# Performance work log

Hardware: AMD Instinct MI355X
Metric: run time of the kernel (lower is better)

## Reference

```python
import jax, jax.numpy as jnp
import numpy as np

N_HEAD = 16
HEAD_DIM = 32          # n_embed // n_head // 2
LAMBDA_INIT = 0.2      # 0.8 - 0.6*exp(-0.3*(layer-1)) with layer=1
ROPE_BASE = 10000.0
EPS = 1e-5


def _rope(x):
    # torchtune RotaryPositionalEmbeddings: interleaved adjacent pairs
    B, T, H, D = x.shape
    half = D // 2
    theta = ROPE_BASE ** (-(jnp.arange(half, dtype=jnp.float32) * 2.0 / D))  # [half]
    ang = jnp.arange(T, dtype=jnp.float32)[:, None] * theta[None, :]         # [T, half]
    cos = jnp.cos(ang)[None, :, None, :]
    sin = jnp.sin(ang)[None, :, None, :]
    xr = x.reshape(B, T, H, half, 2)
    x1, x2 = xr[..., 0], xr[..., 1]
    out = jnp.stack([x1 * cos - x2 * sin, x1 * sin + x2 * cos], axis=-1)
    return out.reshape(B, T, H, D).astype(x.dtype)


def reference(x, W_attn, W_proj, lambda_q1, lambda_k1, lambda_q2, lambda_k2):
    B, T, C = x.shape
    H, D = N_HEAD, HEAD_DIM
    qkv = x @ W_attn                              # [B,T,3C]
    q, k, v = jnp.split(qkv, 3, axis=-1)
    q = _rope(q.reshape(B, T, 2 * H, D)).transpose(0, 2, 1, 3)   # [B,2H,T,D]
    k = _rope(k.reshape(B, T, 2 * H, D)).transpose(0, 2, 1, 3)   # [B,2H,T,D]
    v = v.reshape(B, T, H, 2 * D).transpose(0, 2, 1, 3)          # [B,H,T,2D]

    lam = (jnp.exp(jnp.dot(lambda_q1, lambda_k1))
           - jnp.exp(jnp.dot(lambda_q2, lambda_k2)) + LAMBDA_INIT)

    # causal SDPA over both score paths (2H heads) in one pass, shared V
    scale = 1.0 / jnp.sqrt(jnp.asarray(D, x.dtype))
    scores = jnp.einsum('bhqd,bhkd->bhqk', q, k) * scale         # [B,2H,T,T]
    causal = jnp.tril(jnp.ones((T, T), dtype=bool))
    scores = jnp.where(causal, scores, jnp.finfo(scores.dtype).min)
    probs = jax.nn.softmax(scores, axis=-1)
    vv = jnp.concatenate([v, v], axis=1)                         # [B,2H,T,2D]
    A = jnp.einsum('bhqk,bhkd->bhqd', probs, vv)                 # [B,2H,T,2D]
    A1, A2 = A[:, :H], A[:, H:]

    diff = A1 - lam * A2                                         # [B,H,T,2D]
    # RMSNorm over last dim (2*head_dim), no affine, eps=1e-5
    diff = diff * jax.lax.rsqrt(jnp.mean(diff * diff, axis=-1, keepdims=True) + EPS)
    diff = (1.0 - LAMBDA_INIT) * diff
    out = diff.transpose(0, 2, 1, 3).reshape(B, T, C)
    return out @ W_proj


def setup_inputs() -> dict:
    key = jax.random.key(0)
    ks = jax.random.split(key, 7)
    B, T, C, D = 2, 2048, 1024, HEAD_DIM
    return {
        'x': jax.random.normal(ks[0], (B, T, C), jnp.float32),
        'W_attn': jax.random.normal(ks[1], (C, 3 * C), jnp.float32) * 0.02,
        'W_proj': jax.random.normal(ks[2], (C, C), jnp.float32) * 0.02,
        'lambda_q1': jax.random.normal(ks[3], (D,), jnp.float32) * 0.1,
        'lambda_k1': jax.random.normal(ks[4], (D,), jnp.float32) * 0.1,
        'lambda_q2': jax.random.normal(ks[5], (D,), jnp.float32) * 0.1,
        'lambda_k2': jax.random.normal(ks[6], (D,), jnp.float32) * 0.1,
    }
```

## Files before the change

### kernel.cpp

```cpp
#include <hip/hip_runtime.h>


typedef unsigned short u16;
typedef __bf16 bf16x8 __attribute__((ext_vector_type(8)));
typedef float f32x4 __attribute__((ext_vector_type(4)));
typedef float f32x16 __attribute__((ext_vector_type(16)));
typedef unsigned u32x2 __attribute__((ext_vector_type(2)));

__device__ __forceinline__ u16 f2bf(float f) {
  return __builtin_bit_cast(u16, (__bf16)f);
}
__device__ __forceinline__ float bf2f(u16 u) {
  return (float)__builtin_bit_cast(__bf16, u);
}
__device__ __forceinline__ unsigned pk2(float a, float b) {
  return (unsigned)f2bf(a) | ((unsigned)f2bf(b) << 16);
}

__device__ __forceinline__ void gload16(const u16* g, u16* l) {
  __builtin_amdgcn_global_load_lds(
      (const __attribute__((address_space(1))) unsigned int*)g,
      (__attribute__((address_space(3))) unsigned int*)l, 16, 0, 0);
}

__device__ __forceinline__ void trans_body(const float* __restrict__ in,
                                           u16* __restrict__ out, int R, int Cn,
                                           int bx, int by, float (*tile)[33],
                                           int tx, int ty) {
  const int c0 = bx * 32, r0 = by * 32;
#pragma unroll
  for (int rr = 0; rr < 4; ++rr)
    tile[ty + rr * 8][tx] = in[(size_t)(r0 + ty + rr * 8) * Cn + c0 + tx];
  __syncthreads();
#pragma unroll
  for (int rr = 0; rr < 4; ++rr)
    out[(size_t)(c0 + ty + rr * 8) * R + r0 + tx] = f2bf(tile[tx][ty + rr * 8]);
}

__global__ __launch_bounds__(256) void prep_kernel(
    const float* __restrict__ x, const float* __restrict__ Wa,
    const float* __restrict__ Wp, const float* __restrict__ lq1,
    const float* __restrict__ lk1, const float* __restrict__ lq2,
    const float* __restrict__ lk2, u16* __restrict__ xb, u16* __restrict__ WaT,
    u16* __restrict__ WpT, float2* __restrict__ Tab, float* __restrict__ lamp) {
  __shared__ float tile[32][33];
  const int id = blockIdx.x;
  const int tx = threadIdx.x & 31, ty = threadIdx.x >> 5;
  if (id < 4096) {
    const int i = id * 256 + threadIdx.x;
    float4 v = ((const float4*)x)[i];
    ushort4 o;
    o.x = f2bf(v.x); o.y = f2bf(v.y); o.z = f2bf(v.z); o.w = f2bf(v.w);
    ((ushort4*)xb)[i] = o;
  } else if (id < 7168) {
    const int t = id - 4096;
    trans_body(Wa, WaT, 1024, 3072, t % 96, t / 96, tile, tx, ty);
  } else if (id < 8192) {
    const int t = id - 7168;
    trans_body(Wp, WpT, 1024, 1024, t & 31, t >> 5, tile, tx, ty);
  } else if (id < 8320) {
    const int idx = (id - 8192) * 256 + threadIdx.x;
    const int t = idx >> 4, i = idx & 15;
    const float theta = exp2f(-0.83048202372184059f * (float)i);
    float sn, cs;
    sincosf((float)t * theta, &sn, &cs);
    Tab[idx] = make_float2(cs, sn);
  } else if (threadIdx.x == 0) {
    float d1 = 0.f, d2 = 0.f;
#pragma unroll
    for (int i = 0; i < 32; ++i) {
      d1 += lq1[i] * lk1[i];
      d2 += lq2[i] * lk2[i];
    }
    *lamp = expf(d1) - expf(d2) + 0.2f;
  }
}

__global__ __launch_bounds__(256, 6) void gemm_qkv_kernel(
    const u16* __restrict__ A, const u16* __restrict__ BT,
    u16* __restrict__ Q, u16* __restrict__ K, u16* __restrict__ VT,
    const float2* __restrict__ Tab) {
  const int Kdim = 1024;
  __shared__ u16 SH[12288];
  const int tid = threadIdx.x;
  const int l = tid & 63;
  const int w = tid >> 6;
  const int nwgx = gridDim.x;
  const int lin = blockIdx.x + nwgx * blockIdx.y;
  const int cpx = (nwgx * gridDim.y) >> 3;
  const int swz = (lin & 7) * cpx + (lin >> 3);
  const int bm = swz / nwgx, bn = swz % nwgx;
  const int wm = w >> 1, wn = w & 1;
  const int rowA0 = bm * 64, rowB0 = bn * 128;
  const int r_ = tid >> 2;
  const int s_ = (tid & 3) * 8;
  const u16* Ag = &A[(size_t)(rowA0 + r_) * Kdim + s_];
  const u16* Bg = &BT[(size_t)(rowB0 + r_) * Kdim + s_];
  const size_t rstride = (size_t)64 * Kdim;
  f32x4 acc[2][4] = {};
  gload16(Ag, &SH[tid * 8]);
  gload16(Bg, &SH[2048 + tid * 8]);
  gload16(Bg + rstride, &SH[4096 + tid * 8]);
  __syncthreads();
  int cur = 0;
  for (int t = 0; t < 32; ++t) {
    const u16* Asc = SH + cur * 6144;
    const u16* Bsc = Asc + 2048;
    if (t + 1 < 32) {
      u16* Asn = SH + (cur ^ 1) * 6144;
      const int k1 = (t + 1) * 32;
      gload16(Ag + k1, &Asn[tid * 8]);
      gload16(Bg + k1, &Asn[2048 + tid * 8]);
      gload16(Bg + rstride + k1, &Asn[4096 + tid * 8]);
    }
    bf16x8 a[2], b[4];
#pragma unroll
    for (int i = 0; i < 2; ++i)
      a[i] = *(const bf16x8*)&Asc[(wm * 32 + i * 16 + (l & 15)) * 32 + (l >> 4) * 8];
#pragma unroll
    for (int j = 0; j < 4; ++j)
      b[j] = *(const bf16x8*)&Bsc[(wn * 64 + j * 16 + (l & 15)) * 32 + (l >> 4) * 8];
    __builtin_amdgcn_s_setprio(1);
#pragma unroll
    for (int i = 0; i < 2; ++i)
#pragma unroll
      for (int j = 0; j < 4; ++j)
        acc[i][j] = __builtin_amdgcn_mfma_f32_16x16x32_bf16(a[i], b[j], acc[i][j], 0, 0, 0);
    __builtin_amdgcn_s_setprio(0);
    __syncthreads();
    cur ^= 1;
  }
  const int cr = (l >> 4) * 4;
  const int cc = l & 15;
  const int region = bn >> 3;
  const int b_ = rowA0 >> 11, tb = rowA0 & 2047;
  if (region < 2) {
    const float qsc_ = (region == 0) ? 0.25503486f : 1.0f;
    u16* dst = (region == 0) ? Q : K;
#pragma unroll
    for (int i = 0; i < 2; ++i) {
      const int trow0 = wm * 32 + i * 16 + cr;
#pragma unroll
      for (int j = 0; j < 4; ++j) {
        const int c = (bn & 7) * 128 + wn * 64 + j * 16 + cc;
        const int hh = c >> 5, d = c & 31;
        const int ii = d >> 1;
        const float sgn = (d & 1) ? 1.0f : -1.0f;
        const size_t base = (size_t)(b_ * 32 + hh) * 2048;
#pragma unroll
        for (int r = 0; r < 4; ++r) {
          const int t = tb + trow0 + r;
          const float2 cs = Tab[t * 16 + ii];
          const float xv = acc[i][j][r];
          const float px = __shfl_xor(xv, 1, 64);
          dst[(base + t) * 32 + d] = f2bf((xv * cs.x + sgn * px * cs.y) * qsc_);
        }
      }
    }
  } else {
#pragma unroll
    for (int i = 0; i < 2; ++i) {
      const int t0 = tb + wm * 32 + i * 16 + cr;
#pragma unroll
      for (int j = 0; j < 4; ++j) {
        const int c3 = (bn & 7) * 128 + wn * 64 + j * 16 + cc;
        const int hv = c3 >> 6, dv = c3 & 63;
        ushort4 ov;
        ov.x = f2bf(acc[i][j][0]);
        ov.y = f2bf(acc[i][j][1]);
        ov.z = f2bf(acc[i][j][2]);
        ov.w = f2bf(acc[i][j][3]);
        *(ushort4*)&VT[((size_t)(b_ * 16 + hv) * 64 + dv) * 2048 + t0] = ov;
      }
    }
  }
}

__global__ __launch_bounds__(256) void gemm_out_kernel(
    const u16* __restrict__ A, const u16* __restrict__ BT, float* __restrict__ Cout,
    int Mdim, int Ndim, int Kdim) {
  __shared__ u16 SH[12288];
  const int tid = threadIdx.x;
  const int l = tid & 63;
  const int w = tid >> 6;
  const int nwgx = gridDim.x;
  const int lin = blockIdx.x + nwgx * blockIdx.y;
  const int cpx = (nwgx * gridDim.y) >> 3;
  const int swz = (lin & 7) * cpx + (lin >> 3);
  const int bm = swz / nwgx, bn = swz % nwgx;
  const int wm = w >> 1, wn = w & 1;
  const int rowA0 = bm * 64, rowB0 = bn * 128;
  const int r_ = tid >> 2;
  const int s_ = (tid & 3) * 8;
  const u16* Ag = &A[(size_t)(rowA0 + r_) * Kdim + s_];
  const u16* Bg = &BT[(size_t)(rowB0 + r_) * Kdim + s_];
  const size_t rstride = (size_t)64 * Kdim;
  f32x4 acc[2][4] = {};
  gload16(Ag, &SH[tid * 8]);
  gload16(Bg, &SH[2048 + tid * 8]);
  gload16(Bg + rstride, &SH[4096 + tid * 8]);
  __syncthreads();
  int cur = 0;
  const int nt = Kdim >> 5;
  for (int t = 0; t < nt; ++t) {
    const u16* Asc = SH + cur * 6144;
    const u16* Bsc = Asc + 2048;
    if (t + 1 < nt) {
      u16* Asn = SH + (cur ^ 1) * 6144;
      const int k1 = (t + 1) * 32;
      gload16(Ag + k1, &Asn[tid * 8]);
      gload16(Bg + k1, &Asn[2048 + tid * 8]);
      gload16(Bg + rstride + k1, &Asn[4096 + tid * 8]);
    }
    bf16x8 a[2], b[4];
#pragma unroll
    for (int i = 0; i < 2; ++i)
      a[i] = *(const bf16x8*)&Asc[(wm * 32 + i * 16 + (l & 15)) * 32 + (l >> 4) * 8];
#pragma unroll
    for (int j = 0; j < 4; ++j)
      b[j] = *(const bf16x8*)&Bsc[(wn * 64 + j * 16 + (l & 15)) * 32 + (l >> 4) * 8];
    __builtin_amdgcn_s_setprio(1);
#pragma unroll
    for (int i = 0; i < 2; ++i)
#pragma unroll
      for (int j = 0; j < 4; ++j)
        acc[i][j] = __builtin_amdgcn_mfma_f32_16x16x32_bf16(a[i], b[j], acc[i][j], 0, 0, 0);
    __builtin_amdgcn_s_setprio(0);
    __syncthreads();
    cur ^= 1;
  }
  const int cr = (l >> 4) * 4;
  const int cc = l & 15;
#pragma unroll
  for (int i = 0; i < 2; ++i)
#pragma unroll
    for (int j = 0; j < 4; ++j)
#pragma unroll
      for (int r = 0; r < 4; ++r) {
        const int row = rowA0 + wm * 32 + i * 16 + cr + r;
        const int col = rowB0 + wn * 64 + j * 16 + cc;
        Cout[(size_t)row * Ndim + col] = acc[i][j][r];
      }
}

__global__ __launch_bounds__(256, 4) void attn_kernel(const u16* __restrict__ Q,
                                                      const u16* __restrict__ K,
                                                      const u16* __restrict__ VT,
                                                      u16* __restrict__ PO0,
                                                      u16* __restrict__ PO1,
                                                      float* __restrict__ ML) {
  __shared__ u16 Ks[64 * 34];
  __shared__ u16 Vs[64 * 66];
  __shared__ u16 Os[4 * 32 * 66];
  const int tid = threadIdx.x, l = tid & 63, w = tid >> 6;
  const int pp = blockIdx.x & 7, hf = blockIdx.x >> 3;
  const int h = blockIdx.y, b = blockIdx.z;
  const size_t qkbase = (size_t)(b * 32 + h) * 2048;
  const size_t vtb = (size_t)(b * 16 + (h & 15)) * 64;
  const int lq = l & 31, hi = l >> 5;
  const f32x16 z16 = {};
  const int krow = tid >> 2, ksl = (tid & 3) * 8;
  const int dva = tid >> 3, vsl = (tid & 7) * 8;
  const int dvb = dva + 32;
  const __bf16 one1 = (__bf16)1.0f;
  const bf16x8 ones = {one1, one1, one1, one1, one1, one1, one1, one1};

  for (int halfidx = 0; halfidx < 2; ++halfidx) {
    const int qt = halfidx ? (15 - pp) : pp;
    const int slot = hf ^ halfidx;
    const int s_begin = slot ? (qt + 1) : 0;
    const int s_end = slot ? (2 * qt + 2) : (qt + 1);
    const int q0 = qt * 128;
    const int qw = q0 + w * 32;
    const int q = qw + lq;
    const bf16x8 qf0 = *(const bf16x8*)&Q[(qkbase + q) * 32 + hi * 8];
    const bf16x8 qf1 = *(const bf16x8*)&Q[(qkbase + q) * 32 + 16 + hi * 8];
    f32x16 olo = {}, ohi = {}, lacc = {};
    uint4 kreg = *(const uint4*)&K[(qkbase + s_begin * 64 + krow) * 32 + ksl];
    uint4 vreg0 = *(const uint4*)&VT[(vtb + dva) * 2048 + s_begin * 64 + vsl];
    uint4 vreg1 = *(const uint4*)&VT[(vtb + dvb) * 2048 + s_begin * 64 + vsl];
    for (int s = s_begin; s < s_end; ++s) {
      const int kb = s * 64;
      *(uint4*)&Ks[krow * 34 + ksl] = kreg;
      *(uint4*)&Vs[dva * 66 + vsl] = vreg0;
      *(uint4*)&Vs[dvb * 66 + vsl] = vreg1;
      const int sn = (s + 1 < s_end) ? (s + 1) : s;
      kreg = *(const uint4*)&K[(qkbase + sn * 64 + krow) * 32 + ksl];
      vreg0 = *(const uint4*)&VT[(vtb + dva) * 2048 + sn * 64 + vsl];
      vreg1 = *(const uint4*)&VT[(vtb + dvb) * 2048 + sn * 64 + vsl];
      __syncthreads();
      if (qw + 31 >= kb) {
        f32x16 s0_, s1_;
        {
          const bf16x8 ka0 = *(const bf16x8*)&Ks[lq * 34 + hi * 8];
          const bf16x8 ka1 = *(const bf16x8*)&Ks[lq * 34 + 16 + hi * 8];
          const bf16x8 kc0 = *(const bf16x8*)&Ks[(32 + lq) * 34 + hi * 8];
          const bf16x8 kc1 = *(const bf16x8*)&Ks[(32 + lq) * 34 + 16 + hi * 8];
          __builtin_amdgcn_s_setprio(1);
          s0_ = __builtin_amdgcn_mfma_f32_32x32x16_bf16(ka0, qf0, z16, 0, 0, 0);
          s0_ = __builtin_amdgcn_mfma_f32_32x32x16_bf16(ka1, qf1, s0_, 0, 0, 0);
          s1_ = __builtin_amdgcn_mfma_f32_32x32x16_bf16(kc0, qf0, z16, 0, 0, 0);
          s1_ = __builtin_amdgcn_mfma_f32_32x32x16_bf16(kc1, qf1, s1_, 0, 0, 0);
          __builtin_amdgcn_s_setprio(0);
        }
        const bool nm = (kb + 63 > qw);
        if (nm) {
#pragma unroll
          for (int r = 0; r < 16; ++r) {
            const int kr = (r & 3) + 8 * (r >> 2) + 4 * hi;
            if (kb + kr > q) s0_[r] = -1e30f;
            if (kb + 32 + kr > q) s1_[r] = -1e30f;
          }
        }
#pragma unroll
        for (int r = 0; r < 16; ++r) {
          s0_[r] = __builtin_amdgcn_exp2f(s0_[r]);
          s1_[r] = __builtin_amdgcn_exp2f(s1_[r]);
        }
        unsigned pw[16];
#pragma unroll
        for (int j = 0; j < 8; ++j) {
          pw[j] = pk2(s0_[2 * j], s0_[2 * j + 1]);
          pw[8 + j] = pk2(s1_[2 * j], s1_[2 * j + 1]);
        }
        bf16x8 pa[4];
#pragma unroll
        for (int fidx = 0; fidx < 4; ++fidx) {
          const unsigned* wt = &pw[fidx * 4];
          union { unsigned u[4]; bf16x8 v; } fr;
#if __has_builtin(__builtin_amdgcn_permlane32_swap)
          const u32x2 rA = __builtin_amdgcn_permlane32_swap(wt[0], wt[2], false, false);
          const u32x2 rB = __builtin_amdgcn_permlane32_swap(wt[1], wt[3], false, false);
          fr.u[0] = rA[0]; fr.u[1] = rB[0]; fr.u[2] = rA[1]; fr.u[3] = rB[1];
#else
          const unsigned ua = hi ? wt[0] : wt[2];
          const unsigned ub = hi ? wt[1] : wt[3];
          const unsigned sa = __shfl_xor(ua, 32, 64);
          const unsigned sb = __shfl_xor(ub, 32, 64);
          fr.u[0] = hi ? sa : wt[0];
          fr.u[1] = hi ? sb : wt[1];
          fr.u[2] = hi ? wt[2] : sa;
          fr.u[3] = hi ? wt[3] : sb;
#endif
          pa[fidx] = fr.v;
        }
        __builtin_amdgcn_s_setprio(1);
#pragma unroll
        for (int ks = 0; ks < 4; ++ks) {
          const bf16x8 va = *(const bf16x8*)&Vs[lq * 66 + ks * 16 + hi * 8];
          const bf16x8 vb = *(const bf16x8*)&Vs[(32 + lq) * 66 + ks * 16 + hi * 8];
          olo = __builtin_amdgcn_mfma_f32_32x32x16_bf16(va, pa[ks], olo, 0, 0, 0);
          ohi = __builtin_amdgcn_mfma_f32_32x32x16_bf16(vb, pa[ks], ohi, 0, 0, 0);
          lacc = __builtin_amdgcn_mfma_f32_32x32x16_bf16(ones, pa[ks], lacc, 0, 0, 0);
        }
        __builtin_amdgcn_s_setprio(0);
      }
      __syncthreads();
    }
    const float lsum = lacc[0];
    const float inv = (lsum > 0.f) ? (1.0f / lsum) : 0.f;
    if (hi == 0)
      ML[(size_t)slot * 131072 + qkbase + q] = lsum;
    u16* Ow = &Os[(w * 32 + lq) * 66];
#pragma unroll
    for (int g = 0; g < 4; ++g) {
      const int d0 = 8 * g + 4 * hi;
      *(unsigned*)&Ow[d0] = pk2(olo[4 * g] * inv, olo[4 * g + 1] * inv);
      *(unsigned*)&Ow[d0 + 2] = pk2(olo[4 * g + 2] * inv, olo[4 * g + 3] * inv);
      *(unsigned*)&Ow[32 + d0] = pk2(ohi[4 * g] * inv, ohi[4 * g + 1] * inv);
      *(unsigned*)&Ow[32 + d0 + 2] = pk2(ohi[4 * g + 2] * inv, ohi[4 * g + 3] * inv);
    }
    __syncthreads();
    u16* PO = slot ? PO1 : PO0;
    for (int s2 = tid; s2 < 1024; s2 += 256) {
      const int wv = s2 >> 8, qq = (s2 >> 3) & 31, sl = (s2 & 7) * 8;
      *(uint4*)&PO[(qkbase + q0 + wv * 32 + qq) * 64 + sl] =
          *(const uint4*)&Os[(wv * 32 + qq) * 66 + sl];
    }
    __syncthreads();
  }
}

__global__ __launch_bounds__(256) void diff_rms_kernel(
    const u16* __restrict__ PO0, const u16* __restrict__ PO1,
    const float* __restrict__ ML, const float* __restrict__ lamp,
    u16* __restrict__ Mb) {
  const int g = threadIdx.x >> 5;
  const int dl = (threadIdx.x & 31) * 2;
  const int ridx = blockIdx.x * 8 + g;
  const int b = ridx >> 15, rem = ridx & 32767, h = rem >> 11, t = rem & 2047;
  const float lam = *lamp;
  const size_t row1 = (size_t)(b * 32 + h) * 2048 + t;
  const size_t row2 = (size_t)(b * 32 + 16 + h) * 2048 + t;
  const float lA1 = ML[row1], lB1 = ML[131072 + row1];
  const float lA2 = ML[row2], lB2 = ML[131072 + row2];
  const float i1 = 1.0f / (lA1 + lB1);
  const float wa1 = lA1 * i1, wb1 = lB1 * i1;
  const float i2 = 1.0f / (lA2 + lB2);
  const float wa2 = lA2 * i2, wb2 = lB2 * i2;
  const ushort2 p01 = *(const ushort2*)&PO0[row1 * 64 + dl];
  const ushort2 p11 = *(const ushort2*)&PO1[row1 * 64 + dl];
  const ushort2 p02 = *(const ushort2*)&PO0[row2 * 64 + dl];
  const ushort2 p12 = *(const ushort2*)&PO1[row2 * 64 + dl];
  const float a1x = wa1 * bf2f(p01.x) + wb1 * bf2f(p11.x);
  const float a1y = wa1 * bf2f(p01.y) + wb1 * bf2f(p11.y);
  const float a2x = wa2 * bf2f(p02.x) + wb2 * bf2f(p12.x);
  const float a2y = wa2 * bf2f(p02.y) + wb2 * bf2f(p12.y);
  const float df0 = a1x - lam * a2x;
  const float df1 = a1y - lam * a2y;
  float ss = df0 * df0 + df1 * df1;
  ss += __shfl_xor(ss, 1, 64);
  ss += __shfl_xor(ss, 2, 64);
  ss += __shfl_xor(ss, 4, 64);
  ss += __shfl_xor(ss, 8, 64);
  ss += __shfl_xor(ss, 16, 64);
  const float rms = rsqrtf(ss * (1.0f / 64.0f) + 1e-5f);
  ushort2 o;
  o.x = f2bf(0.8f * df0 * rms);
  o.y = f2bf(0.8f * df1 * rms);
  *(ushort2*)&Mb[((size_t)(b * 2048 + t)) * 1024 + h * 64 + dl] = o;
}

extern "C" void kernel_launch(void* const* d_in, const int* in_sizes, int n_in,
                              void* d_out, int out_size, void* d_ws, size_t ws_size,
                              hipStream_t stream) {
  const float* x = (const float*)d_in[0];
  const float* Wa = (const float*)d_in[1];
  const float* Wp = (const float*)d_in[2];
  const float* lq1 = (const float*)d_in[3];
  const float* lk1 = (const float*)d_in[4];
  const float* lq2 = (const float*)d_in[5];
  const float* lk2 = (const float*)d_in[6];
  if (ws_size < (size_t)(64u << 20)) return;

  char* ws = (char*)d_ws;
  u16* Qarr = (u16*)(ws);
  u16* Karr = (u16*)(ws + (8u << 20));
  u16* VTarr = (u16*)(ws + (16u << 20));
  u16* WpT = (u16*)(ws + (24u << 20));
  char* arena = ws + (26u << 20);
  u16* xb = (u16*)(arena);
  u16* WaT = (u16*)(arena + (8u << 20));
  float2* Tab = (float2*)(arena + (14u << 20));
  u16* PO0 = (u16*)(arena);
  u16* PO1 = (u16*)(arena + (16u << 20));
  float* ML = (float*)(arena + (32u << 20));
  float* lamp = (float*)(arena + (33u << 20));
  u16* Mbuf = Qarr;

  prep_kernel<<<8321, 256, 0, stream>>>(x, Wa, Wp, lq1, lk1, lq2, lk2,
                                        xb, WaT, WpT, Tab, lamp);
  gemm_qkv_kernel<<<dim3(24, 64), 256, 0, stream>>>(xb, WaT, Qarr, Karr, VTarr, Tab);
  attn_kernel<<<dim3(16, 32, 2), 256, 0, stream>>>(Qarr, Karr, VTarr, PO0, PO1, ML);
  diff_rms_kernel<<<8192, 256, 0, stream>>>(PO0, PO1, ML, lamp, Mbuf);
  gemm_out_kernel<<<dim3(8, 64), 256, 0, stream>>>(Mbuf, WpT, (float*)d_out, 4096, 1024, 1024);
}
```

Before: 138.6 us.

## Deepen GEMM LDS pipeline to four stages with explicit vmcnt waits

```diff
diff --git a/kernel.cpp b/kernel.cpp
--- a/kernel.cpp
+++ b/kernel.cpp
@@ -76,12 +76,12 @@
   }
 }
 
-__global__ __launch_bounds__(256, 6) void gemm_qkv_kernel(
+__global__ __launch_bounds__(256, 3) void gemm_qkv_kernel(
     const u16* __restrict__ A, const u16* __restrict__ BT,
     u16* __restrict__ Q, u16* __restrict__ K, u16* __restrict__ VT,
     const float2* __restrict__ Tab) {
   const int Kdim = 1024;
-  __shared__ u16 SH[12288];
+  __shared__ u16 SH[24576];
   const int tid = threadIdx.x;
   const int l = tid & 63;
   const int w = tid >> 6;
@@ -98,21 +98,28 @@
   const u16* Bg = &BT[(size_t)(rowB0 + r_) * Kdim + s_];
   const size_t rstride = (size_t)64 * Kdim;
   f32x4 acc[2][4] = {};
-  gload16(Ag, &SH[tid * 8]);
-  gload16(Bg, &SH[2048 + tid * 8]);
-  gload16(Bg + rstride, &SH[4096 + tid * 8]);
-  __syncthreads();
-  int cur = 0;
-  for (int t = 0; t < 32; ++t) {
-    const u16* Asc = SH + cur * 6144;
+  const int nt = 32;
+#pragma unroll
+  for (int p = 0; p < 3; ++p) {
+    u16* D = SH + p * 6144;
+    const int k1 = p * 32;
+    gload16(Ag + k1, &D[tid * 8]);
+    gload16(Bg + k1, &D[2048 + tid * 8]);
+    gload16(Bg + rstride + k1, &D[4096 + tid * 8]);
+  }
+  asm volatile("s_waitcnt vmcnt(6)" ::: "memory");
+  __builtin_amdgcn_s_barrier();
+  __builtin_amdgcn_sched_barrier(0);
+  for (int t = 0; t < nt; ++t) {
+    if (t + 3 < nt) {
+      u16* D = SH + ((t + 3) & 3) * 6144;
+      const int k1 = (t + 3) * 32;
+      gload16(Ag + k1, &D[tid * 8]);
+      gload16(Bg + k1, &D[2048 + tid * 8]);
+      gload16(Bg + rstride + k1, &D[4096 + tid * 8]);
+    }
+    const u16* Asc = SH + (t & 3) * 6144;
     const u16* Bsc = Asc + 2048;
-    if (t + 1 < 32) {
-      u16* Asn = SH + (cur ^ 1) * 6144;
-      const int k1 = (t + 1) * 32;
-      gload16(Ag + k1, &Asn[tid * 8]);
-      gload16(Bg + k1, &Asn[2048 + tid * 8]);
-      gload16(Bg + rstride + k1, &Asn[4096 + tid * 8]);
-    }
     bf16x8 a[2], b[4];
 #pragma unroll
     for (int i = 0; i < 2; ++i)
@@ -127,8 +134,16 @@
       for (int j = 0; j < 4; ++j)
         acc[i][j] = __builtin_amdgcn_mfma_f32_16x16x32_bf16(a[i], b[j], acc[i][j], 0, 0, 0);
     __builtin_amdgcn_s_setprio(0);
-    __syncthreads();
-    cur ^= 1;
+    if (t + 1 < nt) {
+      if (t + 3 < nt)
+        asm volatile("s_waitcnt vmcnt(6)" ::: "memory");
+      else if (t + 2 < nt)
+        asm volatile("s_waitcnt vmcnt(3)" ::: "memory");
+      else
+        asm volatile("s_waitcnt vmcnt(0)" ::: "memory");
+      __builtin_amdgcn_s_barrier();
+      __builtin_amdgcn_sched_barrier(0);
+    }
   }
   const int cr = (l >> 4) * 4;
   const int cc = l & 15;
@@ -176,10 +191,10 @@
   }
 }
 
-__global__ __launch_bounds__(256) void gemm_out_kernel(
+__global__ __launch_bounds__(256, 3) void gemm_out_kernel(
     const u16* __restrict__ A, const u16* __restrict__ BT, float* __restrict__ Cout,
     int Mdim, int Ndim, int Kdim) {
-  __shared__ u16 SH[12288];
+  __shared__ u16 SH[24576];
   const int tid = threadIdx.x;
   const int l = tid & 63;
   const int w = tid >> 6;
@@ -196,22 +211,28 @@
   const u16* Bg = &BT[(size_t)(rowB0 + r_) * Kdim + s_];
   const size_t rstride = (size_t)64 * Kdim;
   f32x4 acc[2][4] = {};
-  gload16(Ag, &SH[tid * 8]);
-  gload16(Bg, &SH[2048 + tid * 8]);
-  gload16(Bg + rstride, &SH[4096 + tid * 8]);
-  __syncthreads();
-  int cur = 0;
   const int nt = Kdim >> 5;
+#pragma unroll
+  for (int p = 0; p < 3; ++p) {
+    u16* D = SH + p * 6144;
+    const int k1 = p * 32;
+    gload16(Ag + k1, &D[tid * 8]);
+    gload16(Bg + k1, &D[2048 + tid * 8]);
+    gload16(Bg + rstride + k1, &D[4096 + tid * 8]);
+  }
+  asm volatile("s_waitcnt vmcnt(6)" ::: "memory");
+  __builtin_amdgcn_s_barrier();
+  __builtin_amdgcn_sched_barrier(0);
   for (int t = 0; t < nt; ++t) {
-    const u16* Asc = SH + cur * 6144;
+    if (t + 3 < nt) {
+      u16* D = SH + ((t + 3) & 3) * 6144;
+      const int k1 = (t + 3) * 32;
+      gload16(Ag + k1, &D[tid * 8]);
+      gload16(Bg + k1, &D[2048 + tid * 8]);
+      gload16(Bg + rstride + k1, &D[4096 + tid * 8]);
+    }
+    const u16* Asc = SH + (t & 3) * 6144;
     const u16* Bsc = Asc + 2048;
-    if (t + 1 < nt) {
-      u16* Asn = SH + (cur ^ 1) * 6144;
-      const int k1 = (t + 1) * 32;
-      gload16(Ag + k1, &Asn[tid * 8]);
-      gload16(Bg + k1, &Asn[2048 + tid * 8]);
-      gload16(Bg + rstride + k1, &Asn[4096 + tid * 8]);
-    }
     bf16x8 a[2], b[4];
 #pragma unroll
     for (int i = 0; i < 2; ++i)
@@ -226,8 +247,16 @@
       for (int j = 0; j < 4; ++j)
         acc[i][j] = __builtin_amdgcn_mfma_f32_16x16x32_bf16(a[i], b[j], acc[i][j], 0, 0, 0);
     __builtin_amdgcn_s_setprio(0);
-    __syncthreads();
-    cur ^= 1;
+    if (t + 1 < nt) {
+      if (t + 3 < nt)
+        asm volatile("s_waitcnt vmcnt(6)" ::: "memory");
+      else if (t + 2 < nt)
+        asm volatile("s_waitcnt vmcnt(3)" ::: "memory");
+      else
+        asm volatile("s_waitcnt vmcnt(0)" ::: "memory");
+      __builtin_amdgcn_s_barrier();
+      __builtin_amdgcn_sched_barrier(0);
+    }
   }
   const int cr = (l >> 4) * 4;
   const int cc = l & 15;
```

After: 138.9 us. No clear change (+0.2%).
